# Optimization experiments

Measured on AMD Instinct MI355X. Metric: run time of the kernel, lower is better.

The kernel has to match this reference:

```python
import jax, jax.numpy as jnp
import numpy as np

P = 113          # modulus; eq_token = P, vocab = P + 1
D_MODEL = 1024
D_MLP = 4096
BATCH = 16384


def setup_inputs() -> dict:
    key = jax.random.key(0)
    ks = jax.random.split(key, 9)
    return {
        "a": jax.random.randint(ks[0], (BATCH,), 0, P, dtype=jnp.int64 if jax.config.jax_enable_x64 else jnp.int32),
        "b": jax.random.randint(ks[1], (BATCH,), 0, P, dtype=jnp.int64 if jax.config.jax_enable_x64 else jnp.int32),
        "token_embed": jax.random.normal(ks[2], (P + 1, D_MODEL), dtype=jnp.float32),
        "pos_embed": jax.random.normal(ks[3], (3, D_MODEL), dtype=jnp.float32),
        "W_in_w": jax.random.normal(ks[4], (D_MLP, D_MODEL), dtype=jnp.float32) * (1.0 / np.sqrt(D_MODEL)),
        "W_in_b": jax.random.normal(ks[5], (D_MLP,), dtype=jnp.float32) * 0.02,
        "W_out_w": jax.random.normal(ks[6], (D_MODEL, D_MLP), dtype=jnp.float32) * (1.0 / np.sqrt(D_MLP)),
        "W_out_b": jax.random.normal(ks[7], (D_MODEL,), dtype=jnp.float32) * 0.02,
        "unembed_w": jax.random.normal(ks[8], (P, D_MODEL), dtype=jnp.float32) * (1.0 / np.sqrt(D_MODEL)),
    }


def reference(a, b, token_embed, pos_embed, W_in_w, W_in_b, W_out_w, W_out_b, unembed_w):
    # tokens: (batch, 3) = [a, b, eq]
    eq = jnp.full_like(a, P)
    tokens = jnp.stack([a, b, eq], axis=1)
    # embed + positional: (batch, 3, d_model)
    x = token_embed[tokens] + pos_embed[None, :, :]
    # FNet-style mixing: FFT over seq (axis 1), then over d_model (axis 2), real part
    wave = jnp.fft.fft(jnp.fft.fft(x, axis=1), axis=2).real.astype(x.dtype)
    x = x + wave
    # MLP with residual
    h = jax.nn.relu(jnp.einsum('bsd,md->bsm', x, W_in_w) + W_in_b)
    x = x + jnp.einsum('bsm,dm->bsd', h, W_out_w) + W_out_b
    # unembed only the '=' position (index 2)
    logits = jnp.einsum('bd,vd->bv', x[:, 2, :], unembed_w)
    return logits
```

## Files before the change

kernel.cpp:

```cpp
#include <hip/hip_runtime.h>

typedef __attribute__((ext_vector_type(4))) float f32x4;
typedef __attribute__((ext_vector_type(8))) short short8;

#define PMOD 113
#define DM 1024
#define DMLP 4096
#define NBATCH 16384
#define SQRT3_2 0.86602540378443865f
#define CSTEP 6.1359231515425649e-3f
#define LTSTRIDE (12800 * 128)

__device__ __forceinline__ short f2bf(float x) {
    unsigned int u = __builtin_bit_cast(unsigned int, x);
    u += 0x7FFFu + ((u >> 16) & 1u);
    return (short)(u >> 16);
}
__device__ __forceinline__ float bf2f(short s) {
    return __builtin_bit_cast(float, (unsigned int)(unsigned short)s << 16);
}
__device__ __forceinline__ void cvt16(const float* p, short8& o0, short8& o1) {
    #pragma unroll
    for (int c4 = 0; c4 < 4; ++c4) {
        f32x4 v = *(const f32x4*)(p + c4 * 4);
        #pragma unroll
        for (int e = 0; e < 4; ++e) {
            short s = f2bf(v[e]);
            if (c4 < 2) o0[c4 * 4 + e] = s; else o1[(c4 - 2) * 4 + e] = s;
        }
    }
}

__global__ __launch_bounds__(256) void k_prep(
    unsigned short* __restrict__ Fb, unsigned short* __restrict__ V2b,
    unsigned short* __restrict__ Wob,
    const float* __restrict__ E, const float* __restrict__ pos,
    const float* __restrict__ Wo)
{
    __shared__ float smem[64 * 65];
    const int blk = blockIdx.x, tid = threadIdx.x;

    if (blk < 1024) {
        const int f = blk;
        for (int k = tid; k < DM; k += 256) {
            float v;
            if (k <= 512) v = cosf((float)((f * k) & 1023) * CSTEP);
            else          v = sinf((float)((f * (k - 512)) & 1023) * CSTEP);
            Fb[f * DM + k] = (unsigned short)f2bf(v);
        }
    } else if (blk < 1252) {
        const int t = blk - 1024;
        if (t >= 226) {
            for (int k = tid; k < DM; k += 256) V2b[t * DM + k] = 0;
            return;
        }
        float* vc = smem;
        float* vs = smem + 1024;
        if (t < PMOD) {
            const float* e = E + t * DM;
            const float* e2 = E + PMOD * DM;
            for (int d = tid; d < DM; d += 256) {
                float e2v = e2[d] + pos[2 * DM + d];
                vc[d] = e[d] + pos[d] - 0.5f * pos[DM + d] - 0.5f * e2v;
                vs[d] = SQRT3_2 * (pos[DM + d] - e2v);
            }
        } else {
            const float* e = E + (t - PMOD) * DM;
            for (int d = tid; d < DM; d += 256) {
                float x = e[d];
                vc[d] = -0.5f * x;
                vs[d] = SQRT3_2 * x;
            }
        }
        __syncthreads();
        for (int k = tid; k < DM; k += 256) {
            float o;
            if (k == 0)        o = vc[0];
            else if (k < 512)  o = vc[k] + vc[1024 - k];
            else if (k == 512) o = vc[512];
            else               o = vs[k - 512] - vs[1536 - k];
            V2b[t * DM + k] = (unsigned short)f2bf(o);
        }
    } else {
        const int idx = blk - 1252;
        const int m0 = (idx & 63) * 64;
        const int d0 = (idx >> 6) * 64;
        float (*tile)[65] = (float(*)[65])smem;
        #pragma unroll
        for (int it = 0; it < 16; ++it) {
            int i2 = tid + it * 256;
            int r = i2 >> 6, c = i2 & 63;
            tile[c][r] = Wo[(d0 + r) * DMLP + m0 + c];
        }
        __syncthreads();
        #pragma unroll
        for (int it = 0; it < 16; ++it) {
            int i2 = tid + it * 256;
            int r = i2 >> 6, c = i2 & 63;
            Wob[(m0 + r) * DM + d0 + c] = (unsigned short)f2bf(tile[r][c]);
        }
    }
}

template<int MODE>
__device__ __forceinline__ void mfma_body(
    int n0, int row0,
    unsigned short* __restrict__ C1, float* __restrict__ C2,
    const void* __restrict__ Av, const void* __restrict__ B1v,
    const float* __restrict__ B2, const float* __restrict__ bias,
    const float* __restrict__ E, const float* __restrict__ pos,
    const float* __restrict__ bo, short* sA, short* sB)
{
    const int tid = threadIdx.x;
    const int sr = tid >> 2, sq = (tid & 3) * 16;
    const int lane = tid & 63, w = tid >> 6;
    const int wr = w >> 1, wc = w & 1;
    const int lr = lane & 15, lg = lane >> 4;

    const unsigned short* Ab = nullptr; const float* Af = nullptr;
    {
        int r = row0 + sr;
        if (MODE == 2) { if (r < PMOD) Af = (const float*)Av + r * DM; }
        else           { if (r < 228)  Ab = (const unsigned short*)Av + r * DM; }
    }
    const unsigned short* Bb = nullptr; const float* Bf = nullptr;
    {
        int n = n0 + sr;
        if (MODE == 1) {
            if (n < 4096) Bf = (const float*)B1v + n * DM;
            else if (n - 4096 < PMOD) Bf = B2 + (n - 4096) * DM;
        } else {
            Bb = (const unsigned short*)B1v + n * DM;
        }
    }

    f32x4 acc[2][2];
    #pragma unroll
    for (int i = 0; i < 2; ++i)
        #pragma unroll
        for (int j = 0; j < 2; ++j) acc[i][j] = 0.f;

    for (int k0 = 0; k0 < DM; k0 += 64) {
        short8 a0, a1, b0, b1;
        if (MODE == 2) {
            if (Af) cvt16(Af + k0 + sq, a0, a1);
            else { a0 = 0; a1 = 0; }
        } else {
            if (Ab) { a0 = ((const short8*)(Ab + k0 + sq))[0];
                      a1 = ((const short8*)(Ab + k0 + sq))[1]; }
            else { a0 = 0; a1 = 0; }
        }
        if (MODE == 1) {
            if (Bf) cvt16(Bf + k0 + sq, b0, b1);
            else { b0 = 0; b1 = 0; }
        } else {
            b0 = ((const short8*)(Bb + k0 + sq))[0];
            b1 = ((const short8*)(Bb + k0 + sq))[1];
        }
        if (k0) __syncthreads();
        *(short8*)&sA[sr * 72 + sq] = a0;
        *(short8*)&sA[sr * 72 + sq + 8] = a1;
        *(short8*)&sB[sr * 72 + sq] = b0;
        *(short8*)&sB[sr * 72 + sq + 8] = b1;
        __syncthreads();

        #pragma unroll
        for (int ks = 0; ks < 2; ++ks) {
            short8 af[2], bfr[2];
            #pragma unroll
            for (int i = 0; i < 2; ++i)
                af[i] = *(const short8*)&sA[(wr * 32 + i * 16 + lr) * 72 + ks * 32 + lg * 8];
            #pragma unroll
            for (int j = 0; j < 2; ++j)
                bfr[j] = *(const short8*)&sB[(wc * 32 + j * 16 + lr) * 72 + ks * 32 + lg * 8];
            #pragma unroll
            for (int i = 0; i < 2; ++i)
                #pragma unroll
                for (int j = 0; j < 2; ++j)
                    acc[i][j] = __builtin_amdgcn_mfma_f32_16x16x32_bf16(af[i], bfr[j], acc[i][j], 0, 0, 0);
        }
    }

    #pragma unroll
    for (int i = 0; i < 2; ++i) {
        #pragma unroll
        for (int q = 0; q < 4; ++q) {
            int r = row0 + wr * 32 + i * 16 + lg * 4 + q;
            #pragma unroll
            for (int j = 0; j < 2; ++j) {
                int cg = n0 + wc * 32 + j * 16 + lr;
                float v = acc[i][j][q];
                if (MODE == 0) {
                    if (r < 228) {
                        if (r < PMOD) v += E[PMOD * DM + cg] + pos[2 * DM + cg];
                        if (r == 227) v += bo[cg];
                        C1[r * DM + cg] = (unsigned short)f2bf(v);
                    }
                } else if (MODE == 1) {
                    if (r < 228) {
                        if (n0 < 4096) {
                            if (r < PMOD) v += bias[cg];
                            C1[r * DMLP + cg] = (unsigned short)f2bf(v);
                        } else {
                            C2[r * 128 + cg - 4096] = v;
                        }
                    }
                } else {
                    if (r < 128) C1[r * DMLP + cg] = (unsigned short)f2bf(v);
                }
            }
        }
    }
}

__global__ __launch_bounds__(256) void k_m02(
    unsigned short* __restrict__ Tb, unsigned short* __restrict__ Mb,
    const unsigned short* __restrict__ V2b, const unsigned short* __restrict__ Fb,
    const float* __restrict__ U, const unsigned short* __restrict__ Wob,
    const float* __restrict__ E, const float* __restrict__ pos,
    const float* __restrict__ bo)
{
    __shared__ short sA[64 * 72];
    __shared__ short sB[64 * 72];
    const int blk = blockIdx.x;
    if (blk < 64) {
        mfma_body<0>((blk & 15) * 64, (blk >> 4) * 64, Tb, nullptr, V2b, Fb,
                     nullptr, nullptr, E, pos, bo, sA, sB);
    } else {
        int i = blk - 64;
        mfma_body<2>((i & 63) * 64, (i >> 6) * 64, Mb, nullptr, U, Wob,
                     nullptr, nullptr, nullptr, nullptr, nullptr, sA, sB);
    }
}

__global__ __launch_bounds__(256) void k_m1(
    unsigned short* __restrict__ Hb, float* __restrict__ L,
    const unsigned short* __restrict__ Tb, const float* __restrict__ Wi,
    const float* __restrict__ U, const float* __restrict__ bi)
{
    __shared__ short sA[64 * 72];
    __shared__ short sB[64 * 72];
    mfma_body<1>(blockIdx.x * 64, blockIdx.y * 64, Hb, L, Tb, Wi, U, bi,
                 nullptr, nullptr, nullptr, sA, sB);
}

__global__ __launch_bounds__(256) void k_pair_gemm(
    unsigned short* __restrict__ LTp,
    const unsigned short* __restrict__ Hb,
    const unsigned short* __restrict__ Mb,
    const float* __restrict__ L)
{
    __shared__ short hA[64 * 72];
    __shared__ short mB[128 * 72];

    const int tid = threadIdx.x;
    const int a = blockIdx.x;
    const int b0 = blockIdx.y * 64;
    const int kbeg = blockIdx.z * 1024;
    const bool slice0 = (blockIdx.z == 0);
    unsigned short* outp = LTp + (size_t)blockIdx.z * LTSTRIDE;

    const int sr = tid >> 2, sq = (tid & 3) * 16;
    const int brow = b0 + sr;
    const int brc = brow < PMOD ? brow : PMOD - 1;
    const unsigned short* pA = Hb + a * DMLP;
    const unsigned short* pB = Hb + (PMOD + brc) * DMLP;

    const int mv = tid >> 1, mk = (tid & 1) * 32;
    const unsigned short* pM = Mb + mv * DMLP + mk;

    const int lane = tid & 63, w = tid >> 6;
    const int wr = w >> 1, wc = w & 1;
    const int lr = lane & 15, lg = lane >> 4;

    f32x4 acc[2][4];
    #pragma unroll
    for (int i = 0; i < 2; ++i)
        #pragma unroll
        for (int j = 0; j < 4; ++j) acc[i][j] = 0.f;

    short8 rA0[2], rA1[2], rB0[2], rB1[2], rM[2][4];

    #define LOADT(ph, kc)                                              \
        do {                                                           \
            rA0[ph] = ((const short8*)(pA + (kc) + sq))[0];            \
            rA1[ph] = ((const short8*)(pA + (kc) + sq))[1];            \
            rB0[ph] = ((const short8*)(pB + (kc) + sq))[0];            \
            rB1[ph] = ((const short8*)(pB + (kc) + sq))[1];            \
            const short8* s_ = (const short8*)(pM + (kc));             \
            rM[ph][0] = s_[0]; rM[ph][1] = s_[1];                      \
            rM[ph][2] = s_[2]; rM[ph][3] = s_[3];                      \
        } while (0)

    LOADT(0, kbeg);

    for (int k0 = kbeg; k0 < kbeg + 1024; k0 += 128) {
        #pragma unroll
        for (int ph = 0; ph < 2; ++ph) {
            const int kc = k0 + ph * 64;
            if (kc + 64 < kbeg + 1024) LOADT(ph ^ 1, kc + 64);

            short8 u0, u1;
            #pragma unroll
            for (int e = 0; e < 8; ++e) {
                u0[e] = f2bf(fmaxf(bf2f(rA0[ph][e]) + bf2f(rB0[ph][e]), 0.f));
                u1[e] = f2bf(fmaxf(bf2f(rA1[ph][e]) + bf2f(rB1[ph][e]), 0.f));
            }
            if (kc != kbeg) __syncthreads();
            *(short8*)&hA[sr * 72 + sq] = u0;
            *(short8*)&hA[sr * 72 + sq + 8] = u1;
            *(short8*)&mB[mv * 72 + mk] = rM[ph][0];
            *(short8*)&mB[mv * 72 + mk + 8] = rM[ph][1];
            *(short8*)&mB[mv * 72 + mk + 16] = rM[ph][2];
            *(short8*)&mB[mv * 72 + mk + 24] = rM[ph][3];
            __syncthreads();

            #pragma unroll
            for (int ks = 0; ks < 2; ++ks) {
                short8 af[2], bf[4];
                #pragma unroll
                for (int i = 0; i < 2; ++i)
                    af[i] = *(const short8*)&hA[(wr * 32 + i * 16 + lr) * 72 + ks * 32 + lg * 8];
                #pragma unroll
                for (int j = 0; j < 4; ++j)
                    bf[j] = *(const short8*)&mB[(wc * 64 + j * 16 + lr) * 72 + ks * 32 + lg * 8];
                #pragma unroll
                for (int i = 0; i < 2; ++i)
                    #pragma unroll
                    for (int j = 0; j < 4; ++j)
                        acc[i][j] = __builtin_amdgcn_mfma_f32_16x16x32_bf16(af[i], bf[j], acc[i][j], 0, 0, 0);
            }
        }
    }
    #undef LOADT

    const float* La = L + a * 128;
    const float* Lb0 = L + PMOD * 128;
    const float* Lc = L + 227 * 128;
    #pragma unroll
    for (int i = 0; i < 2; ++i) {
        #pragma unroll
        for (int q = 0; q < 4; ++q) {
            int b = b0 + wr * 32 + i * 16 + lg * 4 + q;
            if (b >= PMOD) continue;
            unsigned short* dst = outp + (size_t)(a * PMOD + b) * 128;
            #pragma unroll
            for (int j = 0; j < 4; ++j) {
                int col = wc * 64 + j * 16 + lr;
                float val = acc[i][j][q];
                if (slice0) val += La[col] + Lb0[b * 128 + col] + Lc[col];
                dst[col] = (unsigned short)f2bf(val);
            }
        }
    }
}

__global__ __launch_bounds__(256) void k_gather(
    float* __restrict__ out, const unsigned short* __restrict__ LTp,
    const int* __restrict__ a, const int* __restrict__ b)
{
    int g = blockIdx.x * 256 + threadIdx.x;
    if (g >= NBATCH * PMOD) return;
    unsigned int i = (unsigned)g / 113u;
    unsigned int v = (unsigned)g - i * 113u;
    size_t off = (size_t)((unsigned)a[i] * 113u + (unsigned)b[i]) * 128 + v;
    float s = 0.f;
    #pragma unroll
    for (int z = 0; z < 4; ++z)
        s += bf2f(LTp[(size_t)z * LTSTRIDE + off]);
    out[g] = s;
}

extern "C" void kernel_launch(void* const* d_in, const int* in_sizes, int n_in,
                              void* d_out, int out_size, void* d_ws, size_t ws_size,
                              hipStream_t stream)
{
    const int*   a   = (const int*)d_in[0];
    const int*   b   = (const int*)d_in[1];
    const float* E   = (const float*)d_in[2];
    const float* pos = (const float*)d_in[3];
    const float* Wi  = (const float*)d_in[4];
    const float* bi  = (const float*)d_in[5];
    const float* Wo  = (const float*)d_in[6];
    const float* bo  = (const float*)d_in[7];
    const float* U   = (const float*)d_in[8];
    float* out = (float*)d_out;

    unsigned short* Fb  = (unsigned short*)d_ws;
    unsigned short* V2b = Fb + 1024 * 1024;
    unsigned short* Tb  = V2b + 228 * 1024;
    unsigned short* Hb  = Tb + 228 * 1024;
    unsigned short* Wob = Hb + 228 * 4096;
    unsigned short* Mb  = Wob + 4096 * 1024;
    unsigned short* LTp = Mb + 128 * 4096;
    float* L = (float*)(LTp + 4 * LTSTRIDE);

    k_prep<<<2276, 256, 0, stream>>>(Fb, V2b, Wob, E, pos, Wo);
    k_m02<<<192, 256, 0, stream>>>(Tb, Mb, V2b, Fb, U, Wob, E, pos, bo);
    k_m1<<<dim3(66, 4), 256, 0, stream>>>(Hb, L, Tb, Wi, U, bi);
    k_pair_gemm<<<dim3(PMOD, 2, 4), 256, 0, stream>>>(LTp, Hb, Mb, L);
    k_gather<<<(NBATCH * PMOD + 255) / 256, 256, 0, stream>>>(out, LTp, a, b);

    (void)in_sizes; (void)n_in; (void)out_size; (void)ws_size;
}
```

Baseline: 182.7 us.

## Keep Mb K-slice resident in LDS and loop pair tiles per block

```diff
diff --git a/kernel.cpp b/kernel.cpp
--- a/kernel.cpp
+++ b/kernel.cpp
@@ -10,6 +10,7 @@
 #define SQRT3_2 0.86602540378443865f
 #define CSTEP 6.1359231515425649e-3f
 #define LTSTRIDE (12800 * 128)
+#define NZ 8
 
 __device__ __forceinline__ short f2bf(float x) {
     unsigned int u = __builtin_bit_cast(unsigned int, x);
@@ -244,112 +245,106 @@
                  nullptr, nullptr, nullptr, sA, sB);
 }
 
-__global__ __launch_bounds__(256) void k_pair_gemm(
+__global__ __launch_bounds__(512) void k_pair_gemm(
     unsigned short* __restrict__ LTp,
     const unsigned short* __restrict__ Hb,
     const unsigned short* __restrict__ Mb,
     const float* __restrict__ L)
 {
-    __shared__ short hA[64 * 72];
-    __shared__ short mB[128 * 72];
+    __shared__ short mB[128 * 512];
+    __shared__ short hA[2][64 * 72];
 
     const int tid = threadIdx.x;
-    const int a = blockIdx.x;
-    const int b0 = blockIdx.y * 64;
-    const int kbeg = blockIdx.z * 1024;
-    const bool slice0 = (blockIdx.z == 0);
-    unsigned short* outp = LTp + (size_t)blockIdx.z * LTSTRIDE;
-
-    const int sr = tid >> 2, sq = (tid & 3) * 16;
-    const int brow = b0 + sr;
-    const int brc = brow < PMOD ? brow : PMOD - 1;
-    const unsigned short* pA = Hb + a * DMLP;
-    const unsigned short* pB = Hb + (PMOD + brc) * DMLP;
-
-    const int mv = tid >> 1, mk = (tid & 1) * 32;
-    const unsigned short* pM = Mb + mv * DMLP + mk;
+    const int z = blockIdx.x;
+    const int g = blockIdx.y;
+    const int kbeg = z * 512;
+    const bool slice0 = (z == 0);
+    unsigned short* outp = LTp + (size_t)z * LTSTRIDE;
 
     const int lane = tid & 63, w = tid >> 6;
-    const int wr = w >> 1, wc = w & 1;
+    const int wr = w >> 2, wc = w & 3;
     const int lr = lane & 15, lg = lane >> 4;
-
-    f32x4 acc[2][4];
-    #pragma unroll
-    for (int i = 0; i < 2; ++i)
-        #pragma unroll
-        for (int j = 0; j < 4; ++j) acc[i][j] = 0.f;
-
-    short8 rA0[2], rA1[2], rB0[2], rB1[2], rM[2][4];
-
-    #define LOADT(ph, kc)                                              \
-        do {                                                           \
-            rA0[ph] = ((const short8*)(pA + (kc) + sq))[0];            \
-            rA1[ph] = ((const short8*)(pA + (kc) + sq))[1];            \
-            rB0[ph] = ((const short8*)(pB + (kc) + sq))[0];            \
-            rB1[ph] = ((const short8*)(pB + (kc) + sq))[1];            \
-            const short8* s_ = (const short8*)(pM + (kc));             \
-            rM[ph][0] = s_[0]; rM[ph][1] = s_[1];                      \
-            rM[ph][2] = s_[2]; rM[ph][3] = s_[3];                      \
-        } while (0)
-
-    LOADT(0, kbeg);
-
-    for (int k0 = kbeg; k0 < kbeg + 1024; k0 += 128) {
-        #pragma unroll
-        for (int ph = 0; ph < 2; ++ph) {
-            const int kc = k0 + ph * 64;
-            if (kc + 64 < kbeg + 1024) LOADT(ph ^ 1, kc + 64);
-
-            short8 u0, u1;
-            #pragma unroll
-            for (int e = 0; e < 8; ++e) {
-                u0[e] = f2bf(fmaxf(bf2f(rA0[ph][e]) + bf2f(rB0[ph][e]), 0.f));
-                u1[e] = f2bf(fmaxf(bf2f(rA1[ph][e]) + bf2f(rB1[ph][e]), 0.f));
-            }
-            if (kc != kbeg) __syncthreads();
-            *(short8*)&hA[sr * 72 + sq] = u0;
-            *(short8*)&hA[sr * 72 + sq + 8] = u1;
-            *(short8*)&mB[mv * 72 + mk] = rM[ph][0];
-            *(short8*)&mB[mv * 72 + mk + 8] = rM[ph][1];
-            *(short8*)&mB[mv * 72 + mk + 16] = rM[ph][2];
-            *(short8*)&mB[mv * 72 + mk + 24] = rM[ph][3];
+    const int sr = tid >> 3, sq8 = (tid & 7) * 8;
+
+    {
+        const int l8 = lane * 8;
+        #pragma unroll
+        for (int r = 0; r < 16; ++r) {
+            int v = w * 16 + r;
+            short8 d = *(const short8*)(Mb + v * DMLP + kbeg + l8);
+            *(short8*)&mB[v * 512 + (l8 ^ ((v & 7) << 3))] = d;
+        }
+    }
+
+    for (int u = g; u < 226; u += 32) {
+        const int a = u >> 1;
+        const int b0 = (u & 1) * 64;
+        const int brow = b0 + sr;
+        const int brc = brow < PMOD ? brow : PMOD - 1;
+        const unsigned short* pA = Hb + a * DMLP + kbeg + sq8;
+        const unsigned short* pB = Hb + (PMOD + brc) * DMLP + kbeg + sq8;
+
+        f32x4 acc[2][2];
+        #pragma unroll
+        for (int i = 0; i < 2; ++i)
+            #pragma unroll
+            for (int j = 0; j < 2; ++j) acc[i][j] = 0.f;
+
+        short8 ra = *(const short8*)pA;
+        short8 rb = *(const short8*)pB;
+
+        #pragma unroll
+        for (int t = 0; t < 8; ++t) {
+            short8 ran = ra, rbn = rb;
+            if (t < 7) {
+                ran = *(const short8*)(pA + (t + 1) * 64);
+                rbn = *(const short8*)(pB + (t + 1) * 64);
+            }
+            short8 uu;
+            #pragma unroll
+            for (int e = 0; e < 8; ++e)
+                uu[e] = f2bf(fmaxf(bf2f(ra[e]) + bf2f(rb[e]), 0.f));
+            *(short8*)&hA[t & 1][sr * 72 + sq8] = uu;
             __syncthreads();
 
             #pragma unroll
             for (int ks = 0; ks < 2; ++ks) {
-                short8 af[2], bf[4];
+                short8 af[2], bfr[2];
                 #pragma unroll
                 for (int i = 0; i < 2; ++i)
-                    af[i] = *(const short8*)&hA[(wr * 32 + i * 16 + lr) * 72 + ks * 32 + lg * 8];
+                    af[i] = *(const short8*)&hA[t & 1][(wr * 32 + i * 16 + lr) * 72 + ks * 32 + lg * 8];
                 #pragma unroll
-                for (int j = 0; j < 4; ++j)
-                    bf[j] = *(const short8*)&mB[(wc * 64 + j * 16 + lr) * 72 + ks * 32 + lg * 8];
+                for (int j = 0; j < 2; ++j) {
+                    int v = wc * 32 + j * 16 + lr;
+                    int tk = t * 64 + ks * 32 + lg * 8;
+                    bfr[j] = *(const short8*)&mB[v * 512 + (tk ^ ((v & 7) << 3))];
+                }
                 #pragma unroll
                 for (int i = 0; i < 2; ++i)
                     #pragma unroll
-                    for (int j = 0; j < 4; ++j)
-                        acc[i][j] = __builtin_amdgcn_mfma_f32_16x16x32_bf16(af[i], bf[j], acc[i][j], 0, 0, 0);
-            }
-        }
-    }
-    #undef LOADT
-
-    const float* La = L + a * 128;
-    const float* Lb0 = L + PMOD * 128;
-    const float* Lc = L + 227 * 128;
-    #pragma unroll
-    for (int i = 0; i < 2; ++i) {
-        #pragma unroll
-        for (int q = 0; q < 4; ++q) {
-            int b = b0 + wr * 32 + i * 16 + lg * 4 + q;
-            if (b >= PMOD) continue;
-            unsigned short* dst = outp + (size_t)(a * PMOD + b) * 128;
-            #pragma unroll
-            for (int j = 0; j < 4; ++j) {
-                int col = wc * 64 + j * 16 + lr;
-                float val = acc[i][j][q];
-                if (slice0) val += La[col] + Lb0[b * 128 + col] + Lc[col];
-                dst[col] = (unsigned short)f2bf(val);
+                    for (int j = 0; j < 2; ++j)
+                        acc[i][j] = __builtin_amdgcn_mfma_f32_16x16x32_bf16(af[i], bfr[j], acc[i][j], 0, 0, 0);
+            }
+            ra = ran; rb = rbn;
+        }
+
+        const float* La = L + a * 128;
+        const float* Lb0 = L + PMOD * 128;
+        const float* Lc = L + 227 * 128;
+        #pragma unroll
+        for (int i = 0; i < 2; ++i) {
+            #pragma unroll
+            for (int q = 0; q < 4; ++q) {
+                int b = b0 + wr * 32 + i * 16 + lg * 4 + q;
+                if (b >= PMOD) continue;
+                unsigned short* dst = outp + (size_t)(a * PMOD + b) * 128;
+                #pragma unroll
+                for (int j = 0; j < 2; ++j) {
+                    int col = wc * 32 + j * 16 + lr;
+                    float val = acc[i][j][q];
+                    if (slice0) val += La[col] + Lb0[b * 128 + col] + Lc[col];
+                    dst[col] = (unsigned short)f2bf(val);
+                }
             }
         }
     }
@@ -366,7 +361,7 @@
     size_t off = (size_t)((unsigned)a[i] * 113u + (unsigned)b[i]) * 128 + v;
     float s = 0.f;
     #pragma unroll
-    for (int z = 0; z < 4; ++z)
+    for (int z = 0; z < NZ; ++z)
         s += bf2f(LTp[(size_t)z * LTSTRIDE + off]);
     out[g] = s;
 }
@@ -393,12 +388,12 @@
     unsigned short* Wob = Hb + 228 * 4096;
     unsigned short* Mb  = Wob + 4096 * 1024;
     unsigned short* LTp = Mb + 128 * 4096;
-    float* L = (float*)(LTp + 4 * LTSTRIDE);
+    float* L = (float*)(LTp + NZ * LTSTRIDE);
 
     k_prep<<<2276, 256, 0, stream>>>(Fb, V2b, Wob, E, pos, Wo);
     k_m02<<<192, 256, 0, stream>>>(Tb, Mb, V2b, Fb, U, Wob, E, pos, bo);
     k_m1<<<dim3(66, 4), 256, 0, stream>>>(Hb, L, Tb, Wi, U, bi);
-    k_pair_gemm<<<dim3(PMOD, 2, 4), 256, 0, stream>>>(LTp, Hb, Mb, L);
+    k_pair_gemm<<<dim3(NZ, 32), 512, 0, stream>>>(LTp, Hb, Mb, L);
     k_gather<<<(NBATCH * PMOD + 255) / 256, 256, 0, stream>>>(out, LTp, a, b);
 
     (void)in_sizes; (void)n_in; (void)out_size; (void)ws_size;
```

Result: slower. 199.9 us (+9.4%).
